# Kernel tuning notes

Hardware: AMD Instinct MI355X
Metric: run time of the kernel (lower is better)

## Reference

```python
import jax, jax.numpy as jnp
import numpy as np
from jax import lax

MINUS_INF = -1.0e9
BOS, EOS, PAD = 0, 1, 2
NB_LABELS, MAX_DEPTH, EXTRA = 96, 8, 3
STATE = NB_LABELS * MAX_DEPTH + EXTRA  # 771
B, T = 32, 128


def _init_transitions(key):
    t = jax.random.uniform(key, (STATE, STATE), minval=-0.1, maxval=0.1, dtype=jnp.float32)
    # structural constraints from init_weights()
    t = t.at[:, BOS].set(MINUS_INF)          # nothing transitions into BOS
    t = t.at[EOS, :].set(MINUS_INF)          # nothing leaves EOS
    t = t.at[BOS, NB_LABELS + EXTRA:].set(MINUS_INF)  # BOS only into depth-0 states
    t = t.at[NB_LABELS + EXTRA:, EOS].set(MINUS_INF)  # only depth-0 states into EOS
    t = t.at[PAD, :].set(MINUS_INF)
    t = t.at[NB_LABELS + EXTRA:, PAD].set(MINUS_INF)
    t = t.at[PAD, EOS].set(0.0)
    t = t.at[PAD, PAD].set(0.0)
    return t


def setup_inputs() -> dict:
    key = jax.random.key(0)
    k1, k2, k3 = jax.random.split(key, 3)
    emissions = jax.random.normal(k1, (B, T, STATE), dtype=jnp.float32)
    # valid (non-special) states only, so gold-path scores stay finite
    tags = jax.random.randint(k2, (B, T), EXTRA, STATE, dtype=jnp.int64)
    mask = jnp.ones((B, T), dtype=jnp.float32)
    transitions = _init_transitions(k3)
    return {"emissions": emissions, "tags": tags, "mask": mask, "transitions": transitions}


def _crf_nll(emissions, tags, mask, transitions):
    b, t, s = emissions.shape
    tags = tags.astype(jnp.int32)
    batch_idx = jnp.arange(b)

    # ---- gold path score ----
    first = tags[:, 0]
    scores = transitions[BOS, first] + emissions[batch_idx, 0, first]
    prev, cur = tags[:, :-1], tags[:, 1:]
    e_sc = jnp.take_along_axis(emissions[:, 1:], cur[..., None], axis=2)[..., 0]  # (B,T-1)
    t_sc = transitions[prev, cur]                                                 # (B,T-1)
    scores = scores + jnp.sum((e_sc + t_sc) * mask[:, 1:], axis=1)
    last_idx = mask.sum(axis=1).astype(jnp.int32) - 1
    last_tags = tags[batch_idx, last_idx]
    scores = scores + transitions[last_tags, EOS]

    # ---- log partition: forward algorithm (logsumexp DP over S x S) ----
    alphas0 = transitions[BOS][None, :] + emissions[:, 0]  # (B,S)

    def step(alphas, inp):
        em, m = inp  # em: (B,S), m: (B,)
        # (B,S_prev,1) + (S_prev,S_cur) + (B,1,S_cur) -> logsumexp over S_prev
        new = jax.scipy.special.logsumexp(
            alphas[:, :, None] + transitions[None, :, :] + em[:, None, :], axis=1)
        alphas = jnp.where(m[:, None] > 0, new, alphas)
        return alphas, None

    alphas, _ = lax.scan(step, alphas0,
                         (jnp.swapaxes(emissions[:, 1:], 0, 1), mask[:, 1:].T))
    log_z = jax.scipy.special.logsumexp(alphas + transitions[:, EOS][None, :], axis=1)

    # nll = -sum(score - logZ)
    return -jnp.sum(scores - log_z)


def reference(emissions, tags, mask, transitions):
    return _crf_nll(emissions, tags, mask, transitions)
```

## Files before the change

### kernel.cpp

```cpp
#include <hip/hip_runtime.h>
#include <math.h>

typedef unsigned long long u64;

static constexpr int S    = 771;
static constexpr int Tn   = 128;
static constexpr int Bn   = 32;
static constexpr int BOSs = 0;
static constexpr int EOSs = 1;

static constexpr int JPAD  = 832;
static constexpr int JB    = 13;
static constexpr int ROWS  = 64;
static constexpr int NQ    = 4;
static constexpr int SL    = JPAD / NQ;
static constexpr int CH    = SL / 16;
static constexpr int EBLK  = NQ * CH * ROWS * 16;
static constexpr int ETOT  = JB * EBLK;
static constexpr int XSTR  = 224;
static constexpr float CB  = 8.0f;
static constexpr float C0V = 4.5f;

__device__ __forceinline__ float wave_max_bfly(float v) {
    #pragma unroll
    for (int off = 32; off > 0; off >>= 1) v = fmaxf(v, __shfl_xor(v, off));
    return v;
}
__device__ __forceinline__ float wave_sum_f(float v) {
    #pragma unroll
    for (int off = 32; off > 0; off >>= 1) v += __shfl_down(v, off);
    return v;
}

__device__ __forceinline__ u64 ald64(const u64* p) {
    return __hip_atomic_load((u64*)p, __ATOMIC_RELAXED, __HIP_MEMORY_SCOPE_AGENT);
}
__device__ __forceinline__ void ast64(u64* p, u64 v) {
    __hip_atomic_store(p, v, __ATOMIC_RELAXED, __HIP_MEMORY_SCOPE_AGENT);
}
__device__ __forceinline__ u64 pack(unsigned tag, unsigned payload) {
    return ((u64)tag << 32) | (u64)payload;
}

#if __has_builtin(__builtin_amdgcn_sdot4)
__device__ __forceinline__ int dot4i(unsigned a, unsigned b, int c) {
    return __builtin_amdgcn_sdot4((int)a, (int)b, c, false);
}
#else
__device__ __forceinline__ int dot4i(unsigned a, unsigned b, int c) {
    c += (int)(a & 0xff)         * (int)(b & 0xff);
    c += (int)((a >> 8) & 0xff)  * (int)((b >> 8) & 0xff);
    c += (int)((a >> 16) & 0xff) * (int)((b >> 16) & 0xff);
    c += (int)((a >> 24) & 0xff) * (int)((b >> 24) & 0xff);
    return c;
}
#endif

extern "C" __global__ void build_tabs(const float* __restrict__ trans,
                                      unsigned char* __restrict__ eswz,
                                      float* __restrict__ eteos) {
    int idx = blockIdx.x * blockDim.x + threadIdx.x;
    if (idx < JPAD)
        eteos[idx] = (idx < S) ? __expf(trans[idx * S + EOSs]) : 0.f;
    if (idx >= ETOT) return;
    int e = idx & 15;
    int q = idx >> 4;
    int lane = q & 63;  q >>= 6;
    int kk = q % 13;
    int h  = q / 13;
    int w  = h & 3, jblk = h >> 2;
    int i = w * SL + kk * 16 + e;
    int j = jblk * ROWS + lane;
    float v = 0.f;
    if (i < S && j < S) v = 115.f * __expf(trans[i * S + j]);
    int q8 = (int)(v + 0.5f);
    if (q8 > 127) q8 = 127;
    eswz[idx] = (unsigned char)q8;
}

__device__ __forceinline__ void publish(u64* W, int jblk, unsigned tag,
                                        float af, float C, int lane) {
    float xf = fminf(127.f, 127.f * __expf(af - C));
    int xi = (int)(xf + 0.5f);
    int b0 = __shfl(xi, (4 * lane) & 63);
    int b1 = __shfl(xi, (4 * lane + 1) & 63);
    int b2 = __shfl(xi, (4 * lane + 2) & 63);
    int b3 = __shfl(xi, (4 * lane + 3) & 63);
    unsigned payload = (unsigned)b0 | ((unsigned)b1 << 8)
                     | ((unsigned)b2 << 16) | ((unsigned)b3 << 24);
    float mc = wave_max_bfly(af);
    u64* base = W + 17 * jblk;
    if (lane < 16)  ast64(base + lane, pack(tag, payload));
    if (lane == 16) ast64(base + 16,   pack(tag, __float_as_uint(mc)));
}

extern "C" __global__ __launch_bounds__(256, 2)
void crf_fwd(const float* __restrict__ em, const float* __restrict__ mask,
             const float* __restrict__ trans, const int* __restrict__ tags,
             const unsigned char* __restrict__ eswz,
             const float* __restrict__ eteos,
             u64* __restrict__ xb, float* __restrict__ out) {
    const int jblk = blockIdx.x, b = blockIdx.y;
    const int tid = threadIdx.x, lane = tid & 63, w = tid >> 6;
    const int j0 = jblk * ROWS;
    const int bw = (13 * w) / 4;
    const int lo = 52 * w - 16 * bw;

    __shared__ __align__(16) unsigned char Elds[EBLK];
    __shared__ __align__(16) unsigned pq[NQ][SL / 4];
    __shared__ int   part[2][NQ][ROWS];
    __shared__ float cshare;
    __shared__ float redv[4], redm[4];

    const float KLOG  = __logf(115.f * 127.f);
    const float KL127 = __logf(127.f);

    {
        const unsigned char* gsrc = eswz + (size_t)jblk * EBLK;
        #pragma unroll
        for (int it = 0; it < EBLK / 4096; ++it)
            *(float4*)(Elds + it * 4096 + tid * 16) =
                *(const float4*)(gsrc + it * 4096 + tid * 16);
    }

    float af = -INFINITY, Cuse = C0V;
    if (w == 0) {
        int j = j0 + lane;
        if (j < S) af = trans[BOSs * S + j] + em[((size_t)b * Tn + 0) * S + j];
        publish(xb + ((size_t)0 * Bn + b) * XSTR, jblk, 0u, af, C0V, lane);
    }

    const bool pollmax = (w == 0) && (lane < JB);

    for (int t = 1; t < Tn; ++t) {
        const u64* R = xb + ((size_t)((t - 1) & 1) * Bn + b) * XSTR;
        u64*       W = xb + ((size_t)((t    ) & 1) * Bn + b) * XSTR;

        float emv = 0.f, mval = 0.f;
        if (w == 0) {
            const int j = j0 + lane;
            if (j < S) emv = em[((size_t)b * Tn + t) * S + j];
            mval = mask[b * Tn + t];
        }

        const unsigned tg = (unsigned)(t - 1);
        const u64* pd = R + 17 * (bw + (lane >> 4)) + (lane & 15);
        const u64* pm = R + 17 * lane + 16;
        u64 qd = 0, qm = 0;
        bool okd = false, okm = !pollmax;
        do {
            if (!okd) { qd = ald64(pd); okd = ((unsigned)(qd >> 32) == tg); }
            if (!okm) { qm = ald64(pm); okm = ((unsigned)(qm >> 32) == tg); }
        } while (__any((!okd) | (!okm)));

        if (lane >= lo && lane < lo + 52) pq[w][lane - lo] = (unsigned)qd;

        float Cnew = 0.f;
        if (w == 0) {
            float mv = (lane < JB) ? __uint_as_float((unsigned)qm) : -INFINITY;
            Cnew = wave_max_bfly(mv) + CB;
        }

        int acc = 0;
        const uint4* E4 = (const uint4*)Elds;
        const uint4* P4 = (const uint4*)pq[w];
        #pragma unroll
        for (int kk = 0; kk < CH; ++kk) {
            const uint4 ev = E4[(w * CH + kk) * 64 + lane];
            const uint4 pv = P4[kk];
            acc = dot4i(ev.x, pv.x, acc);
            acc = dot4i(ev.y, pv.y, acc);
            acc = dot4i(ev.z, pv.z, acc);
            acc = dot4i(ev.w, pv.w, acc);
        }
        part[t & 1][w][lane] = acc;
        __syncthreads();

        if (w == 0) {
            int s4 = part[t & 1][0][lane] + part[t & 1][1][lane]
                   + part[t & 1][2][lane] + part[t & 1][3][lane];
            float nv = Cuse - KLOG + __logf((float)s4) + emv;
            af = (mval > 0.f) ? nv : af;
            publish(W, jblk, (unsigned)t, af, Cnew, lane);
            if (lane == 0) cshare = Cnew;
            Cuse = Cnew;
        }
    }

    if (jblk == 0) {
        const u64* R = xb + ((size_t)((Tn - 1) & 1) * Bn + b) * XSTR;
        const unsigned tg = (unsigned)(Tn - 1);
        const bool act = (tid < JB * 16);
        u64 q = 0;
        bool ok = !act;
        while (true) {
            if (!ok) {
                q = ald64(R + 17 * (tid >> 4) + (tid & 15));
                ok = ((unsigned)(q >> 32) == tg);
            }
            if (__syncthreads_and(ok)) break;
        }
        float lsum = 0.f;
        if (act) {
            unsigned pv = (unsigned)q;
            int base = 4 * tid;
            lsum = (float)(pv & 0xff)         * eteos[base]
                 + (float)((pv >> 8)  & 0xff) * eteos[base + 1]
                 + (float)((pv >> 16) & 0xff) * eteos[base + 2]
                 + (float)((pv >> 24) & 0xff) * eteos[base + 3];
        }
        float mk = 0.f, val = 0.f;
        if (tid < Tn) {
            mk = mask[b * Tn + tid];
            if (tid > 0) {
                int cur  = tags[b * Tn + tid];
                int prev = tags[b * Tn + tid - 1];
                val = (em[((size_t)b * Tn + tid) * S + cur]
                       + trans[prev * S + cur]) * mk;
            }
        }
        lsum = wave_sum_f(lsum);
        float vs = wave_sum_f(val);
        float ms = wave_sum_f(mk);
        if (lane == 0) { redv[w] = vs; redm[w] = ms; part[0][0][w] = 0; }
        if (lane == 1) part[1][0][w] = __float_as_int(lsum);
        __syncthreads();
        if (tid == 0) {
            float tot = __int_as_float(part[1][0][0]) + __int_as_float(part[1][0][1])
                      + __int_as_float(part[1][0][2]) + __int_as_float(part[1][0][3]);
            float logz = cshare - KL127 + __logf(tot);
            float msum = redm[0] + redm[1] + redm[2] + redm[3];
            int last   = (int)(msum + 0.5f) - 1;
            int first  = tags[b * Tn];
            int lastt  = tags[b * Tn + last];
            float score = redv[0] + redv[1] + redv[2] + redv[3]
                        + trans[BOSs * S + first]
                        + em[((size_t)b * Tn) * S + first]
                        + trans[lastt * S + EOSs];
            atomicAdd(out, -(score - logz));
        }
    }
}

extern "C" void kernel_launch(void* const* d_in, const int* in_sizes, int n_in,
                              void* d_out, int out_size, void* d_ws, size_t ws_size,
                              hipStream_t stream) {
    const float* em    = (const float*)d_in[0];
    const int*   tags  = (const int*)d_in[1];
    const float* mask  = (const float*)d_in[2];
    const float* trans = (const float*)d_in[3];
    float* out = (float*)d_out;

    char* ws = (char*)d_ws;
    size_t off = 0;
    unsigned char* eswz = (unsigned char*)(ws + off);
    off += (size_t)ETOT;
    off = (off + 255) & ~(size_t)255;
    float* eteos = (float*)(ws + off); off += JPAD * sizeof(float);
    off = (off + 255) & ~(size_t)255;
    u64* xb = (u64*)(ws + off);        off += (size_t)2 * Bn * XSTR * sizeof(u64);

    (void)hipMemsetAsync(out, 0, sizeof(float), stream);

    build_tabs<<<(ETOT + 255) / 256, 256, 0, stream>>>(trans, eswz, eteos);
    crf_fwd<<<dim3(JB, Bn), 256, 0, stream>>>(em, mask, trans, tags, eswz,
                                              eteos, xb, out);
}
```

Before: 391.3 us.

## Give each wave its own 16-column slice with register-resident weights, drop block barrier

Each of the four waves now owns 16 output states and splits the previous-state dimension across its four 16-lane quarters. Quantized transition weights are held in registers instead of LDS, and partial sums are combined with cross-lane shuffles. This removes the per-step __syncthreads and the shared-memory partial reduction. Every wave now publishes and polls independently, with a new exchange-buffer layout that carries a max per wave. The cost is four times more global polling traffic per block, more publishers, and higher register pressure.

```diff
diff --git a/kernel.cpp b/kernel.cpp
--- a/kernel.cpp
+++ b/kernel.cpp
@@ -2,6 +2,7 @@
 #include <math.h>
 
 typedef unsigned long long u64;
+typedef unsigned int u32;
 
 static constexpr int S    = 771;
 static constexpr int Tn   = 128;
@@ -11,13 +12,13 @@
 
 static constexpr int JPAD  = 832;
 static constexpr int JB    = 13;
-static constexpr int ROWS  = 64;
-static constexpr int NQ    = 4;
-static constexpr int SL    = JPAD / NQ;
-static constexpr int CH    = SL / 16;
-static constexpr int EBLK  = NQ * CH * ROWS * 16;
+static constexpr int NW    = 4;
+static constexpr int KK    = 13;
+static constexpr int NDATA = JB * 16;
+static constexpr int NMAX  = JB * NW;
+static constexpr int XSTR  = 272;
+static constexpr int EBLK  = NW * KK * 64 * 16;
 static constexpr int ETOT  = JB * EBLK;
-static constexpr int XSTR  = 224;
 static constexpr float CB  = 8.0f;
 static constexpr float C0V = 4.5f;
 
@@ -64,13 +65,13 @@
         eteos[idx] = (idx < S) ? __expf(trans[idx * S + EOSs]) : 0.f;
     if (idx >= ETOT) return;
     int e = idx & 15;
-    int q = idx >> 4;
-    int lane = q & 63;  q >>= 6;
-    int kk = q % 13;
-    int h  = q / 13;
+    int r = idx >> 4;
+    int lane = r & 63;  r >>= 6;
+    int kk = r % 13;
+    int h  = r / 13;
     int w  = h & 3, jblk = h >> 2;
-    int i = w * SL + kk * 16 + e;
-    int j = jblk * ROWS + lane;
+    int i = (lane >> 4) * 208 + kk * 16 + e;
+    int j = jblk * 64 + w * 16 + (lane & 15);
     float v = 0.f;
     if (i < S && j < S) v = 115.f * __expf(trans[i * S + j]);
     int q8 = (int)(v + 0.5f);
@@ -78,7 +79,7 @@
     eswz[idx] = (unsigned char)q8;
 }
 
-__device__ __forceinline__ void publish(u64* W, int jblk, unsigned tag,
+__device__ __forceinline__ void publish(u64* Wp, int jblk, int w, unsigned tag,
                                         float af, float C, int lane) {
     float xf = fminf(127.f, 127.f * __expf(af - C));
     int xi = (int)(xf + 0.5f);
@@ -89,9 +90,8 @@
     unsigned payload = (unsigned)b0 | ((unsigned)b1 << 8)
                      | ((unsigned)b2 << 16) | ((unsigned)b3 << 24);
     float mc = wave_max_bfly(af);
-    u64* base = W + 17 * jblk;
-    if (lane < 16)  ast64(base + lane, pack(tag, payload));
-    if (lane == 16) ast64(base + 16,   pack(tag, __float_as_uint(mc)));
+    if (lane < 4)  ast64(Wp + jblk * 16 + 4 * w + lane, pack(tag, payload));
+    if (lane == 4) ast64(Wp + NDATA + jblk * NW + w,    pack(tag, __float_as_uint(mc)));
 }
 
 extern "C" __global__ __launch_bounds__(256, 2)
@@ -102,107 +102,96 @@
              u64* __restrict__ xb, float* __restrict__ out) {
     const int jblk = blockIdx.x, b = blockIdx.y;
     const int tid = threadIdx.x, lane = tid & 63, w = tid >> 6;
-    const int j0 = jblk * ROWS;
-    const int bw = (13 * w) / 4;
-    const int lo = 52 * w - 16 * bw;
-
-    __shared__ __align__(16) unsigned char Elds[EBLK];
-    __shared__ __align__(16) unsigned pq[NQ][SL / 4];
-    __shared__ int   part[2][NQ][ROWS];
+    const int q  = lane >> 4;
+    const int jl = lane & 15;
+    const int j  = jblk * 64 + w * 16 + jl;
+
+    __shared__ u32 strip[NW][NDATA];
     __shared__ float cshare;
-    __shared__ float redv[4], redm[4];
+    __shared__ float redv[NW], redm[NW], redl[NW];
 
     const float KLOG  = __logf(115.f * 127.f);
     const float KL127 = __logf(127.f);
 
+    float af = -INFINITY, Cuse = C0V;
+    if (j < S) af = trans[BOSs * S + j] + em[((size_t)b * Tn + 0) * S + j];
+    publish(xb + ((size_t)0 * Bn + b) * XSTR, jblk, w, 0u, af, C0V, lane);
+
+    uint4 ereg[KK];
     {
-        const unsigned char* gsrc = eswz + (size_t)jblk * EBLK;
+        const uint4* src = (const uint4*)eswz + ((size_t)(jblk * NW + w) * KK) * 64 + lane;
         #pragma unroll
-        for (int it = 0; it < EBLK / 4096; ++it)
-            *(float4*)(Elds + it * 4096 + tid * 16) =
-                *(const float4*)(gsrc + it * 4096 + tid * 16);
+        for (int kk = 0; kk < KK; ++kk) ereg[kk] = src[kk * 64];
     }
 
-    float af = -INFINITY, Cuse = C0V;
-    if (w == 0) {
-        int j = j0 + lane;
-        if (j < S) af = trans[BOSs * S + j] + em[((size_t)b * Tn + 0) * S + j];
-        publish(xb + ((size_t)0 * Bn + b) * XSTR, jblk, 0u, af, C0V, lane);
+    const bool act = (lane < 52);
+
+    for (int t = 1; t < Tn; ++t) {
+        const u64* R  = xb + ((size_t)((t - 1) & 1) * Bn + b) * XSTR;
+        u64*       Wp = xb + ((size_t)((t    ) & 1) * Bn + b) * XSTR;
+
+        float emv = 0.f;
+        if (j < S) emv = em[((size_t)b * Tn + t) * S + j];
+        float mval = mask[b * Tn + t];
+
+        const unsigned tg = (unsigned)(t - 1);
+        const u64* pd = R + 4 * lane;
+        const u64* pm = R + NDATA + lane;
+        u64 d0 = 0, d1 = 0, d2 = 0, d3 = 0, qm = 0;
+        bool o0 = !act, o1 = !act, o2 = !act, o3 = !act, om = !act;
+        do {
+            if (!o0) { d0 = ald64(pd + 0); o0 = ((unsigned)(d0 >> 32) == tg); }
+            if (!o1) { d1 = ald64(pd + 1); o1 = ((unsigned)(d1 >> 32) == tg); }
+            if (!o2) { d2 = ald64(pd + 2); o2 = ((unsigned)(d2 >> 32) == tg); }
+            if (!o3) { d3 = ald64(pd + 3); o3 = ((unsigned)(d3 >> 32) == tg); }
+            if (!om) { qm = ald64(pm);     om = ((unsigned)(qm >> 32) == tg); }
+        } while (__any((!o0) | (!o1) | (!o2) | (!o3) | (!om)));
+
+        if (act) {
+            u64 w01 = ((u64)(u32)d1 << 32) | (u64)(u32)d0;
+            u64 w23 = ((u64)(u32)d3 << 32) | (u64)(u32)d2;
+            *(u64*)&strip[w][4 * lane]     = w01;
+            *(u64*)&strip[w][4 * lane + 2] = w23;
+        }
+
+        float mv = act ? __uint_as_float((u32)qm) : -INFINITY;
+        float Cnew = wave_max_bfly(mv) + CB;
+
+        int a0 = 0, a1 = 0, a2 = 0, a3 = 0;
+        const uint4* P4 = (const uint4*)&strip[w][0] + q * KK;
+        #pragma unroll
+        for (int kk = 0; kk < KK; ++kk) {
+            const uint4 pv = P4[kk];
+            a0 = dot4i(ereg[kk].x, pv.x, a0);
+            a1 = dot4i(ereg[kk].y, pv.y, a1);
+            a2 = dot4i(ereg[kk].z, pv.z, a2);
+            a3 = dot4i(ereg[kk].w, pv.w, a3);
+        }
+        int s4 = (a0 + a1) + (a2 + a3);
+        s4 += __shfl_xor(s4, 16);
+        s4 += __shfl_xor(s4, 32);
+
+        float nv = Cuse - KLOG + __logf((float)s4) + emv;
+        af = (mval > 0.f) ? nv : af;
+        publish(Wp, jblk, w, (unsigned)t, af, Cnew, lane);
+        Cuse = Cnew;
     }
 
-    const bool pollmax = (w == 0) && (lane < JB);
-
-    for (int t = 1; t < Tn; ++t) {
-        const u64* R = xb + ((size_t)((t - 1) & 1) * Bn + b) * XSTR;
-        u64*       W = xb + ((size_t)((t    ) & 1) * Bn + b) * XSTR;
-
-        float emv = 0.f, mval = 0.f;
-        if (w == 0) {
-            const int j = j0 + lane;
-            if (j < S) emv = em[((size_t)b * Tn + t) * S + j];
-            mval = mask[b * Tn + t];
-        }
-
-        const unsigned tg = (unsigned)(t - 1);
-        const u64* pd = R + 17 * (bw + (lane >> 4)) + (lane & 15);
-        const u64* pm = R + 17 * lane + 16;
-        u64 qd = 0, qm = 0;
-        bool okd = false, okm = !pollmax;
-        do {
-            if (!okd) { qd = ald64(pd); okd = ((unsigned)(qd >> 32) == tg); }
-            if (!okm) { qm = ald64(pm); okm = ((unsigned)(qm >> 32) == tg); }
-        } while (__any((!okd) | (!okm)));
-
-        if (lane >= lo && lane < lo + 52) pq[w][lane - lo] = (unsigned)qd;
-
-        float Cnew = 0.f;
-        if (w == 0) {
-            float mv = (lane < JB) ? __uint_as_float((unsigned)qm) : -INFINITY;
-            Cnew = wave_max_bfly(mv) + CB;
-        }
-
-        int acc = 0;
-        const uint4* E4 = (const uint4*)Elds;
-        const uint4* P4 = (const uint4*)pq[w];
-        #pragma unroll
-        for (int kk = 0; kk < CH; ++kk) {
-            const uint4 ev = E4[(w * CH + kk) * 64 + lane];
-            const uint4 pv = P4[kk];
-            acc = dot4i(ev.x, pv.x, acc);
-            acc = dot4i(ev.y, pv.y, acc);
-            acc = dot4i(ev.z, pv.z, acc);
-            acc = dot4i(ev.w, pv.w, acc);
-        }
-        part[t & 1][w][lane] = acc;
-        __syncthreads();
-
-        if (w == 0) {
-            int s4 = part[t & 1][0][lane] + part[t & 1][1][lane]
-                   + part[t & 1][2][lane] + part[t & 1][3][lane];
-            float nv = Cuse - KLOG + __logf((float)s4) + emv;
-            af = (mval > 0.f) ? nv : af;
-            publish(W, jblk, (unsigned)t, af, Cnew, lane);
-            if (lane == 0) cshare = Cnew;
-            Cuse = Cnew;
-        }
-    }
+    if (w == 0 && lane == 0) cshare = Cuse;
 
     if (jblk == 0) {
         const u64* R = xb + ((size_t)((Tn - 1) & 1) * Bn + b) * XSTR;
         const unsigned tg = (unsigned)(Tn - 1);
-        const bool act = (tid < JB * 16);
-        u64 q = 0;
-        bool ok = !act;
+        const bool tact = (tid < NDATA);
+        u64 qd = 0;
+        bool ok = !tact;
         while (true) {
-            if (!ok) {
-                q = ald64(R + 17 * (tid >> 4) + (tid & 15));
-                ok = ((unsigned)(q >> 32) == tg);
-            }
+            if (!ok) { qd = ald64(R + tid); ok = ((unsigned)(qd >> 32) == tg); }
             if (__syncthreads_and(ok)) break;
         }
         float lsum = 0.f;
-        if (act) {
-            unsigned pv = (unsigned)q;
+        if (tact) {
+            unsigned pv = (unsigned)qd;
             int base = 4 * tid;
             lsum = (float)(pv & 0xff)         * eteos[base]
                  + (float)((pv >> 8)  & 0xff) * eteos[base + 1]
@@ -222,12 +211,11 @@
         lsum = wave_sum_f(lsum);
         float vs = wave_sum_f(val);
         float ms = wave_sum_f(mk);
-        if (lane == 0) { redv[w] = vs; redm[w] = ms; part[0][0][w] = 0; }
-        if (lane == 1) part[1][0][w] = __float_as_int(lsum);
+        if (lane == 0) { redv[w] = vs; redm[w] = ms; }
+        if (lane == 1) redl[w] = lsum;
         __syncthreads();
         if (tid == 0) {
-            float tot = __int_as_float(part[1][0][0]) + __int_as_float(part[1][0][1])
-                      + __int_as_float(part[1][0][2]) + __int_as_float(part[1][0][3]);
+            float tot  = redl[0] + redl[1] + redl[2] + redl[3];
             float logz = cshare - KL127 + __logf(tot);
             float msum = redm[0] + redm[1] + redm[2] + redm[3];
             int last   = (int)(msum + 0.5f) - 1;
```

Result: slower. 501.0 us (+28.0%).
